# Kernel optimization log

Measured on AMD Instinct MI355X. Metric: run time of the kernel, lower is better.

## Reference

```python
import jax, jax.numpy as jnp
import numpy as np

B, L, C, H, K, P = 64, 2048, 128, 128, 64, 336
NUM_BLOCKS = 4
EPS = 1e-5


def _revin_norm(x):
    mean = jnp.mean(x, axis=1, keepdims=True)
    std = jnp.sqrt(jnp.var(x, axis=1, keepdims=True) + EPS)
    return (x - mean) / std, mean, std


def _bn(x, gamma, beta, ch_axis):
    # training-mode BatchNorm1d: stats over all axes except ch_axis
    axes = tuple(i for i in range(x.ndim) if i != ch_axis)
    mean = jnp.mean(x, axis=axes, keepdims=True)
    var = jnp.var(x, axis=axes, keepdims=True)
    shp = [1] * x.ndim
    shp[ch_axis] = -1
    return (x - mean) / jnp.sqrt(var + EPS) * gamma.reshape(shp) + beta.reshape(shp)


def _mixer_block(x, bn_t_g, bn_t_b, lin_t_w, lin_t_b, bn_f_g, bn_f_b,
                 lin_f1_w, lin_f1_b, lin_f2_w, lin_f2_b):
    # timestep mixer: BN treats seq dim as channels, Linear over seq dim
    y = _bn(x, bn_t_g, bn_t_b, 1)                       # [B,L,C]
    y = jnp.swapaxes(y, 1, 2)                           # [B,C,L]
    y = jax.nn.gelu(y @ lin_t_w + lin_t_b, approximate=False)
    y = jnp.swapaxes(y, 1, 2)
    x = x + y
    # feature mixer: BN over channel dim, 2-layer MLP over features
    y = jnp.swapaxes(x, 1, 2)                           # [B,C,L]
    y = _bn(y, bn_f_g, bn_f_b, 1)
    y = jnp.swapaxes(y, 1, 2)                           # [B,L,C]
    y = jax.nn.gelu(y @ lin_f1_w + lin_f1_b, approximate=False)
    y = y @ lin_f2_w + lin_f2_b
    return x + y


def _forward(x, bern_u, cluster_embeds, wq_w, wq_b, wk_w, wk_b, wv_w, wv_b,
             cm_w1, cm_b1, cm_w2, cm_b2, tm_w1, tm_b1, tm_w2, tm_b2,
             bn_t_g, bn_t_b, lin_t_w, lin_t_b, bn_f_g, bn_f_b,
             lin_f1_w, lin_f1_b, lin_f2_w, lin_f2_b, out_w, out_b):
    xn, _, _ = _revin_norm(x)                           # [B,L,C]
    # channel MLP -> token embeddings h_i
    h = jax.nn.relu(xn @ cm_w1 + cm_b1) @ cm_w2 + cm_b2  # [B,L,H]
    # cosine-similarity soft routing to codebook
    hn = h / (jnp.linalg.norm(h, axis=-1, keepdims=True) + 1e-8)
    cn = cluster_embeds / (jnp.linalg.norm(cluster_embeds, axis=-1, keepdims=True) + 1e-8)
    p = jax.nn.softmax(jnp.einsum('blh,kh->blk', hn, cn), axis=-1)   # [B,L,K]
    M = (bern_u < p).astype(x.dtype)                    # bernoulli sample via external uniforms
    # exp-attention between cluster queries and token keys, masked by M
    Q = cluster_embeds @ wq_w + wq_b                    # [K,H]
    Km = h @ wk_w + wk_b                                # [B,L,H]
    V = h @ wv_w + wv_b                                 # [B,L,H]
    scores = jnp.einsum('kh,blh->bkl', Q, Km) / jnp.sqrt(jnp.asarray(H, x.dtype))
    aw = jax.nn.softmax(jnp.exp(scores) * jnp.swapaxes(M, 1, 2), axis=-1)  # [B,K,L]
    ao = jnp.einsum('bkl,blh->bkh', aw, V)              # [B,K,H]
    upd = ao * jnp.mean(p, axis=1)[:, :, None]          # prob-weighted cluster update
    new_cluster_embeds = jnp.mean(upd, axis=0)          # [K,H] (EMA-style copy target)
    # temporal module on channel embeddings
    h2 = jax.nn.relu(h @ tm_w1 + tm_b1) @ tm_w2 + tm_b2  # [B,L,H], H==C
    z, mean2, std2 = _revin_norm(h2)                    # second 'norm' overwrites stats
    for _ in range(NUM_BLOCKS):
        z = _mixer_block(z, bn_t_g, bn_t_b, lin_t_w, lin_t_b,
                         bn_f_g, bn_f_b, lin_f1_w, lin_f1_b, lin_f2_w, lin_f2_b)
    y = jnp.swapaxes(jnp.swapaxes(z, 1, 2) @ out_w + out_b, 1, 2)    # [B,P,C]
    y = y * std2 + mean2                                # denorm with second-call stats
    return y, new_cluster_embeds


def setup_inputs() -> dict:
    key = jax.random.key(0)
    ks = iter(jax.random.split(key, 40))

    def lin_w(fan_in, shape):
        return jax.random.uniform(next(ks), shape, jnp.float32, -1.0, 1.0) / np.sqrt(fan_in).astype(np.float32)

    return {
        'x': jax.random.normal(next(ks), (B, L, C), jnp.float32),
        'bern_u': jax.random.uniform(next(ks), (B, L, K), jnp.float32),
        'cluster_embeds': jax.random.normal(next(ks), (K, H), jnp.float32),
        'wq_w': lin_w(H, (H, H)), 'wq_b': lin_w(H, (H,)),
        'wk_w': lin_w(H, (H, H)), 'wk_b': lin_w(H, (H,)),
        'wv_w': lin_w(H, (H, H)), 'wv_b': lin_w(H, (H,)),
        'cm_w1': lin_w(C, (C, H)), 'cm_b1': lin_w(C, (H,)),
        'cm_w2': lin_w(H, (H, H)), 'cm_b2': lin_w(H, (H,)),
        'tm_w1': lin_w(H, (H, H)), 'tm_b1': lin_w(H, (H,)),
        'tm_w2': lin_w(H, (H, H)), 'tm_b2': lin_w(H, (H,)),
        'bn_t_g': jnp.ones((L,), jnp.float32), 'bn_t_b': jnp.zeros((L,), jnp.float32),
        'lin_t_w': lin_w(L, (L, L)), 'lin_t_b': lin_w(L, (L,)),
        'bn_f_g': jnp.ones((C,), jnp.float32), 'bn_f_b': jnp.zeros((C,), jnp.float32),
        'lin_f1_w': lin_w(C, (C, H)), 'lin_f1_b': lin_w(C, (H,)),
        'lin_f2_w': lin_w(H, (H, C)), 'lin_f2_b': lin_w(H, (C,)),
        'out_w': lin_w(L, (L, P)), 'out_b': lin_w(L, (P,)),
    }


def reference(x, bern_u, cluster_embeds, wq_w, wq_b, wk_w, wk_b, wv_w, wv_b,
              cm_w1, cm_b1, cm_w2, cm_b2, tm_w1, tm_b1, tm_w2, tm_b2,
              bn_t_g, bn_t_b, lin_t_w, lin_t_b, bn_f_g, bn_f_b,
              lin_f1_w, lin_f1_b, lin_f2_w, lin_f2_b, out_w, out_b):
    return _forward(x, bern_u, cluster_embeds, wq_w, wq_b, wk_w, wk_b, wv_w, wv_b,
                    cm_w1, cm_b1, cm_w2, cm_b2, tm_w1, tm_b1, tm_w2, tm_b2,
                    bn_t_g, bn_t_b, lin_t_w, lin_t_b, bn_f_g, bn_f_b,
                    lin_f1_w, lin_f1_b, lin_f2_w, lin_f2_b, out_w, out_b)
```

## Files before the change

### kernel.cpp

```cpp
#include <hip/hip_runtime.h>
#include <math.h>

#define BB 64
#define LL 2048
#define CC 128
#define HH 128
#define KK 64
#define PP 336
#define EPSf 1e-5f

typedef __attribute__((ext_vector_type(8))) short short8v;
typedef __attribute__((ext_vector_type(4))) float float4v;

__device__ inline ushort f2bf(float f) {
    union { float f; unsigned u; } v; v.f = f;
    unsigned r = (v.u + 0x7FFFu + ((v.u >> 16) & 1u)) >> 16;
    return (ushort)r;
}
__device__ inline float bf2f(ushort h) {
    union { unsigned u; float f; } v; v.u = ((unsigned)h) << 16;
    return v.f;
}

__device__ inline float fast_gelu(float v) {
// ... 432 lines not shown
                    for (int nf = 0; nf < 4; ++nf)
                        acc2[mf][nf] = __builtin_amdgcn_mfma_f32_16x16x32_bf16(
                            ah[mf], bl[nf], acc2[mf][nf], 0, 0, 0);
                #pragma unroll
                for (int mf = 0; mf < 4; ++mf)
                    #pragma unroll
                    for (int nf = 0; nf < 4; ++nf)
                        acc2[mf][nf] = __builtin_amdgcn_mfma_f32_16x16x32_bf16(
                            al[mf], bh[nf], acc2[mf][nf], 0, 0, 0);
            }
        }
    }

    int rbase = kq * 4;
    float rs_[4][4];
    float rq_[4][4];
    float cs_[4], cq_[4];
    if (EP2 == 1 || EP2 == 3) {
        #pragma unroll
        for (int a = 0; a < 4; ++a)
            #pragma unroll
            for (int b = 0; b < 4; ++b) { rs_[a][b] = 0.f; rq_[a][b] = 0.f; }
    }
    if (EP2 == 2) {
        #pragma unroll
        for (int a = 0; a < 4; ++a) { cs_[a] = 0.f; cq_[a] = 0.f; }
    }
    #pragma unroll
    for (int nf = 0; nf < 4; ++nf) {
        int n = wn + nf * 16 + col;
        float bn = b2v[n];
        #pragma unroll
        for (int mf = 0; mf < 4; ++mf) {
            #pragma unroll
            for (int r = 0; r < 4; ++r) {
                int m = m0 + wm + mf * 16 + rbase + r;
                float v = acc2[mf][nf][r] + bn;
                if (ACT2 == 1) v = fmaxf(v, 0.f);
                if (ACT2 == 2) v = fast_gelu(v);
                if (EP2 == 1) {
                    float fin = Out[(size_t)m * 128 + n] + v;
                    Out[(size_t)m * 128 + n] = fin;
                    rs_[mf][r] += fin;
                    rq_[mf][r] += fin * fin;
                } else {
                    Out[(size_t)m * 128 + n] = v;
                    if (EP2 == 2) { cs_[nf] += v; cq_[nf] += v * v; }
                    if (EP2 == 3) rq_[mf][r] += v * v;
                }
            }
        }
    }
    if (EP2 == 1) {
        #pragma unroll
        for (int mf = 0; mf < 4; ++mf)
            #pragma unroll
            for (int r = 0; r < 4; ++r) {
                float s = rs_[mf][r], q = rq_[mf][r];
                #pragma unroll
                for (int o = 1; o <= 8; o <<= 1) {
                    s += __shfl_xor(s, o);
                    q += __shfl_xor(q, o);
                }
                rs_[mf][r] = s; rq_[mf][r] = q;
            }
        __syncthreads();
        float* sred = (float*)&Xhi[0][0];
        float* qred = sred + 256;
        if (col == 0) {
            #pragma unroll
            for (int mf = 0; mf < 4; ++mf)
                #pragma unroll
                for (int r = 0; r < 4; ++r) {
                    int row = wm + mf * 16 + kq * 4 + r;
                    sred[row * 2 + (wn >> 6)] = rs_[mf][r];
                    qred[row * 2 + (wn >> 6)] = rq_[mf][r];
                }
        }
        __syncthreads();
        if (tid < 128) {
            rsum[(size_t)m0 + tid] = sred[tid * 2] + sred[tid * 2 + 1];
            rsq[(size_t)m0 + tid]  = qred[tid * 2] + qred[tid * 2 + 1];
        }
    }
    if (EP2 == 3) {
        #pragma unroll
        for (int mf = 0; mf < 4; ++mf)
            #pragma unroll
            for (int r = 0; r < 4; ++r) {
                float q = rq_[mf][r];
                #pragma unroll
                for (int o = 1; o <= 8; o <<= 1) q += __shfl_xor(q, o);
                rq_[mf][r] = q;
            }
        __syncthreads();
        float* qred = (float*)&Xhi[0][0];
        if (col == 0) {
            #pragma unroll
            for (int mf = 0; mf < 4; ++mf)
                #pragma unroll
                for (int r = 0; r < 4; ++r) {
                    int row = wm + mf * 16 + kq * 4 + r;
                    qred[row * 2 + (wn >> 6)] = rq_[mf][r];
                }
        }
        __syncthreads();
        if (tid < 128)
            rsq[(size_t)m0 + tid] = qred[tid * 2] + qred[tid * 2 + 1];
    }
    if (EP2 == 2) {
        #pragma unroll
        for (int nf = 0; nf < 4; ++nf) {
            #pragma unroll
            for (int o = 16; o <= 32; o <<= 1) {
                cs_[nf] += __shfl_xor(cs_[nf], o);
                cq_[nf] += __shfl_xor(cq_[nf], o);
            }
        }
        __syncthreads();
        float* colS = (float*)&Xhi[0][0];
        float* colQ = colS + 256;
        if (kq == 0) {
            #pragma unroll
            for (int nf = 0; nf < 4; ++nf) {
                int n = wn + nf * 16 + col;
                colS[(wm >> 6) * 128 + n] = cs_[nf];
                colQ[(wm >> 6) * 128 + n] = cq_[nf];
            }
        }
        __syncthreads();
        if (tid < 128) {
            rsum[(size_t)blockIdx.x * 256 + tid] = colS[tid] + colS[128 + tid];
            rsum[(size_t)blockIdx.x * 256 + 128 + tid] = colQ[tid] + colQ[128 + tid];
        }
    }
}

__global__ void wsplit_kernel(const float* __restrict__ W, ushort* __restrict__ Whi,
                              ushort* __restrict__ Wlo) {
    __shared__ float t[32][33];
    int k0 = blockIdx.x * 32, n0 = blockIdx.y * 32;
    int tx = threadIdx.x, ty = threadIdx.y;
    for (int i = ty; i < 32; i += 8)
        t[i][tx] = W[(size_t)(k0 + i) * 128 + n0 + tx];
    __syncthreads();
    for (int i = ty; i < 32; i += 8) {
        float v = t[tx][i];
        ushort h = f2bf(v);
        Whi[(size_t)(n0 + i) * 128 + k0 + tx] = h;
        Wlo[(size_t)(n0 + i) * 128 + k0 + tx] = f2bf(v - bf2f(h));
    }
}

__global__ __launch_bounds__(512)
void mfma_ts_kernel(const ushort* __restrict__ A, const ushort* __restrict__ W,
                    const float* __restrict__ bias, float* Z,
                    int nx, int nwg, float* __restrict__ bnfP) {
    extern __shared__ __align__(16) ushort smem[];
    float (*Ol)[132] = (float(*)[132])smem;

    int bid = blockIdx.x;
    int cpx = nwg >> 3;
    int swz = (bid & 7) * cpx + (bid >> 3);
    int n0 = (swz % nx) * 128;
    int m0 = (swz / nx) * 128;

    int tid = threadIdx.x;
    int w = tid >> 6, lane = tid & 63;
    int wm = (w >> 1) * 32, wn = (w & 1) * 64;
    int col = lane & 15, kq = lane >> 4;
    int srow = lane >> 3;
    int scol = ((lane & 7) ^ srow) << 3;
    int xr = (col & 7) << 4;

    float4v acc[2][4];
    #pragma unroll
    for (int i = 0; i < 2; ++i)
        #pragma unroll
        for (int j = 0; j < 4; ++j) acc[i][j] = (float4v){0.f, 0.f, 0.f, 0.f};

    const int kTiles = LL >> 6;

    auto stage = [&](int kt2, int bsel) {
        ushort* Ab = smem + bsel * 16384;
        ushort* Bb = Ab + 8192;
        int kb = kt2 << 6;
        #pragma unroll
        for (int it = 0; it < 2; ++it) {
            int rb = w * 16 + it * 8;
            async16(A + (size_t)(m0 + rb + srow) * LL + kb + scol, Ab + (rb << 6));
            async16(W + (size_t)(n0 + rb + srow) * LL + kb + scol, Bb + (rb << 6));
        }
    };

    stage(0, 0);
    stage(1, 1);
    int cur = 0;
    for (int kt = 0; kt < kTiles; ++kt) {
        if (kt + 1 < kTiles)
            asm volatile("s_waitcnt vmcnt(4)" ::: "memory");
        else
            asm volatile("s_waitcnt vmcnt(0)" ::: "memory");
        __builtin_amdgcn_s_barrier();
        __builtin_amdgcn_sched_barrier(0);
        if (kt + 2 < kTiles) {
            int nb = cur + 2; if (nb >= 3) nb -= 3;
            stage(kt + 2, nb);
        }
        const ushort* Ac = smem + cur * 16384;
        const ushort* Bc = Ac + 8192;
        __builtin_amdgcn_s_setprio(1);
        #pragma unroll
        for (int ksub = 0; ksub < 2; ++ksub) {
            int cswz = (((ksub << 6) + (kq << 4)) ^ xr) >> 1;
            short8v af[2], bf[4];
            af[0] = *(const short8v*)(Ac + (wm + col) * 64 + cswz);
            af[1] = *(const short8v*)(Ac + (wm + 16 + col) * 64 + cswz);
            #pragma unroll
            for (int nf = 0; nf < 4; ++nf)
                bf[nf] = *(const short8v*)(Bc + (wn + nf * 16 + col) * 64 + cswz);
            #pragma unroll
            for (int mf = 0; mf < 2; ++mf)
                #pragma unroll
                for (int nf = 0; nf < 4; ++nf)
                    acc[mf][nf] = __builtin_amdgcn_mfma_f32_16x16x32_bf16(
                        af[mf], bf[nf], acc[mf][nf], 0, 0, 0);
        }
        __builtin_amdgcn_s_setprio(0);
        ++cur; if (cur == 3) cur = 0;
    }

    int b = m0 >> 7;
    float cs[8], cq[8];
    #pragma unroll
    for (int j = 0; j < 8; ++j) { cs[j] = 0.f; cq[j] = 0.f; }
    #pragma unroll
    for (int q = 0; q < 4; ++q) {
        __syncthreads();
        #pragma unroll
        for (int nf = 0; nf < 4; ++nf) {
            int gnl = wn + nf * 16;
            if ((gnl >> 5) != q) continue;
            int gn = n0 + gnl + col;
            float bn = bias[gn];
            int nl = gnl - q * 32 + col;
            #pragma unroll
            for (int mf = 0; mf < 2; ++mf)
                #pragma unroll
                for (int r = 0; r < 4; ++r) {
                    float v = acc[mf][nf][r] + bn;
                    v = fast_gelu(v);
                    Ol[nl][wm + mf * 16 + kq * 4 + r] = v;
                }
        }
        __syncthreads();
        int nloc = tid >> 4, c0 = (tid & 15) * 8;
        int gn = n0 + q * 32 + nloc;
        float* zr = Z + ((size_t)b * LL + gn) * CC + c0;
        #pragma unroll
        for (int i = 0; i < 2; ++i) {
            float4 v = *(float4*)&Ol[nloc][c0 + i * 4];
            float4 o = *(float4*)(zr + i * 4);
            v.x += o.x; v.y += o.y; v.z += o.z; v.w += o.w;
            *(float4*)(zr + i * 4) = v;
            cs[i * 4 + 0] += v.x; cs[i * 4 + 1] += v.y;
            cs[i * 4 + 2] += v.z; cs[i * 4 + 3] += v.w;
            cq[i * 4 + 0] += v.x * v.x; cq[i * 4 + 1] += v.y * v.y;
            cq[i * 4 + 2] += v.z * v.z; cq[i * 4 + 3] += v.w * v.w;
        }
    }
    __syncthreads();
    float* sred = (float*)smem;
    float* qred = sred + 4096;
    int rrow = tid >> 4, cb = (tid & 15) * 8;
    #pragma unroll
    for (int j = 0; j < 8; ++j) {
        sred[rrow * 128 + cb + j] = cs[j];
        qred[rrow * 128 + cb + j] = cq[j];
    }
    __syncthreads();
    if (tid < 128) {
        float a = 0.f;
        for (int r = 0; r < 32; ++r) a += sred[r * 128 + tid];
        bnfP[(size_t)bid * 256 + tid] = a;
    } else if (tid < 256) {
        int c = tid - 128;
        float a = 0.f;
        for (int r = 0; r < 32; ++r) a += qred[r * 128 + c];
        bnfP[(size_t)bid * 256 + 128 + c] = a;
    }
}

template <int EPM>
__global__ __launch_bounds__(256)
void mfma_gemm_kernel(const ushort* __restrict__ A, const ushort* __restrict__ W,
                      const float* __restrict__ bias, float* Z,
                      int N, int Kd, int LDO, int nx, int nwg,
                      const float* __restrict__ epS, const float* __restrict__ epM,
                      float* __restrict__ bnfP) {
    __shared__ __align__(16) ushort smem[32768];
    float (*Ol)[132] = (float(*)[132])smem;

    int bid = blockIdx.x;
    int cpx = nwg >> 3;
    int swz = (bid & 7) * cpx + (bid >> 3);
    int n0 = (swz % nx) * 128;
    int m0 = (swz / nx) * 128;

    int tid = threadIdx.x;
    int w = tid >> 6, lane = tid & 63;
    int wm = (w >> 1) * 64, wn = (w & 1) * 64;
    int col = lane & 15, kq = lane >> 4;

    int srow = lane >> 3;
    int scol = ((lane & 7) ^ srow) << 3;
    int xr = (col & 7) << 4;

    float4v acc[4][4];
    #pragma unroll
    for (int i = 0; i < 4; ++i)
        #pragma unroll
        for (int j = 0; j < 4; ++j) acc[i][j] = (float4v){0.f, 0.f, 0.f, 0.f};

    int kTiles = Kd >> 6;

    #pragma unroll
    for (int it = 0; it < 4; ++it) {
        int rb = (w << 5) + (it << 3);
        async16(A + (size_t)(m0 + rb + srow) * Kd + scol, smem + (rb << 6));
    }
    #pragma unroll
    for (int it = 0; it < 4; ++it) {
        int rb = (w << 5) + (it << 3);
        async16(W + (size_t)(n0 + rb + srow) * Kd + scol, smem + 8192 + (rb << 6));
    }
    __syncthreads();

    for (int kt = 0; kt < kTiles; ++kt) {
        int cur = kt & 1;
        ushort* Ac = smem + (cur << 14);
        ushort* Bc = Ac + 8192;
        if (kt + 1 < kTiles) {
            ushort* An = smem + ((cur ^ 1) << 14);
            ushort* Bn = An + 8192;
            int kb = (kt + 1) << 6;
            #pragma unroll
            for (int it = 0; it < 4; ++it) {
                int rb = (w << 5) + (it << 3);
                async16(A + (size_t)(m0 + rb + srow) * Kd + kb + scol, An + (rb << 6));
            }
            #pragma unroll
            for (int it = 0; it < 4; ++it) {
                int rb = (w << 5) + (it << 3);
                async16(W + (size_t)(n0 + rb + srow) * Kd + kb + scol, Bn + (rb << 6));
            }
        }
        __builtin_amdgcn_s_setprio(1);
        #pragma unroll
        for (int ksub = 0; ksub < 2; ++ksub) {
            int cswz = (((ksub << 6) + (kq << 4)) ^ xr) >> 1;
            short8v af[4], bf[4];
            #pragma unroll
            for (int mf = 0; mf < 4; ++mf)
                af[mf] = *(const short8v*)(Ac + (wm + mf * 16 + col) * 64 + cswz);
            #pragma unroll
            for (int nf = 0; nf < 4; ++nf)
                bf[nf] = *(const short8v*)(Bc + (wn + nf * 16 + col) * 64 + cswz);
            #pragma unroll
            for (int mf = 0; mf < 4; ++mf)
                #pragma unroll
                for (int nf = 0; nf < 4; ++nf)
                    acc[mf][nf] = __builtin_amdgcn_mfma_f32_16x16x32_bf16(
                        af[mf], bf[nf], acc[mf][nf], 0, 0, 0);
        }
        __builtin_amdgcn_s_setprio(0);
        __syncthreads();
    }

    int b = m0 >> 7;
    float cs[16], cq[16];
    if (EPM == 1) {
        #pragma unroll
        for (int k2 = 0; k2 < 16; ++k2) { cs[k2] = 0.f; cq[k2] = 0.f; }
    }
    #pragma unroll
    for (int q = 0; q < 4; ++q) {
        __syncthreads();
        #pragma unroll
        for (int nf = 0; nf < 4; ++nf) {
            int gnl = wn + nf * 16;
            if ((gnl >> 5) != q) continue;
            int gn = n0 + gnl + col;
            float bn = (EPM == 2 && gn >= N) ? 0.f : bias[gn];
            int nl = gnl - q * 32 + col;
            #pragma unroll
            for (int mf = 0; mf < 4; ++mf) {
                #pragma unroll
                for (int r = 0; r < 4; ++r) {
                    float v = acc[mf][nf][r] + bn;
                    if (EPM == 1) v = fast_gelu(v);
                    Ol[nl][wm + mf * 16 + kq * 4 + r] = v;
                }
            }
        }
        __syncthreads();
        int nloc = tid >> 3, c0 = (tid & 7) * 16;
        int gn = n0 + q * 32 + nloc;
        if ((EPM == 2 || EPM == 3) && gn >= N) continue;
        float* zr;
        if (EPM == 3)
            zr = Z + (((size_t)(m0 >> 11) * 64 + gn) * 2048) + (m0 & 2047) + c0;
        else
            zr = Z + ((size_t)b * LDO + gn) * CC + c0;
        #pragma unroll
        for (int i = 0; i < 4; ++i) {
            float4 v = *(float4*)&Ol[nloc][c0 + i * 4];
            if (EPM == 1) {
                float4 o = *(float4*)(zr + i * 4);
                v.x += o.x; v.y += o.y; v.z += o.z; v.w += o.w;
                *(float4*)(zr + i * 4) = v;
                cs[i * 4 + 0] += v.x; cs[i * 4 + 1] += v.y;
                cs[i * 4 + 2] += v.z; cs[i * 4 + 3] += v.w;
                cq[i * 4 + 0] += v.x * v.x; cq[i * 4 + 1] += v.y * v.y;
                cq[i * 4 + 2] += v.z * v.z; cq[i * 4 + 3] += v.w * v.w;
            } else if (EPM == 2) {
                int mb = m0 + c0 + i * 4;
                float4 s4 = *(const float4*)(epS + mb);
                float4 m4 = *(const float4*)(epM + mb);
                v.x = v.x * s4.x + m4.x; v.y = v.y * s4.y + m4.y;
                v.z = v.z * s4.z + m4.z; v.w = v.w * s4.w + m4.w;
                *(float4*)(zr + i * 4) = v;
            } else {
                *(float4*)(zr + i * 4) = v;
            }
        }
    }
    if (EPM == 1) {
        __syncthreads();
        float* sred = (float*)smem;
        float* qred = sred + 4096;
        int rrow = tid >> 3, cb = (tid & 7) * 16;
// ... 161 lines not shown
void awh_part_kernel(const float* __restrict__ AWs, const float* __restrict__ hmat,
                     float* __restrict__ part) {
    __shared__ float AT[32][64];
    __shared__ float VT[32][128];
    int b = blockIdx.y, sp = blockIdx.x;
    int tid = threadIdx.x;
    int tx = tid & 15, ty = tid >> 4;
    float acc[4][8] = {};
    const float* Ab = AWs + (size_t)b * KK * LL + sp * 512;
    const float* Vb = hmat + ((size_t)b * LL + sp * 512) * HH;
    for (int lt = 0; lt < 512; lt += 32) {
        __syncthreads();
        #pragma unroll
        for (int it = 0; it < 2; ++it) {
            int q = tid + it * 256;
            int row = q >> 3;
            int lq = (q & 7) << 2;
            float4 v = *(const float4*)(Ab + (size_t)row * LL + lt + lq);
            AT[lq][row] = v.x; AT[lq + 1][row] = v.y;
            AT[lq + 2][row] = v.z; AT[lq + 3][row] = v.w;
        }
        #pragma unroll
        for (int it = 0; it < 4; ++it) {
            int q = tid + it * 256;
            int lr = q >> 5;
            int hc = (q & 31) << 2;
            *(float4*)&VT[lr][hc] = *(const float4*)(Vb + (size_t)(lt + lr) * HH + hc);
        }
        __syncthreads();
        #pragma unroll
        for (int l = 0; l < 32; ++l) {
            float av[4], vv[8];
            *(float4*)&av[0] = *(const float4*)&AT[l][ty * 4];
            *(float4*)&vv[0] = *(const float4*)&VT[l][tx * 4];
            *(float4*)&vv[4] = *(const float4*)&VT[l][64 + tx * 4];
            #pragma unroll
            for (int i = 0; i < 4; ++i)
                #pragma unroll
                for (int j = 0; j < 8; ++j)
                    acc[i][j] = fmaf(av[i], vv[j], acc[i][j]);
        }
    }
    #pragma unroll
    for (int i = 0; i < 4; ++i) {
        int k = ty * 4 + i;
        #pragma unroll
        for (int jj = 0; jj < 8; jj += 4) {
            int h = (jj ? 64 + tx * 4 : tx * 4);
            float o[4];
            #pragma unroll
            for (int j = 0; j < 4; ++j) o[j] = acc[i][jj + j];
            *(float4*)(part + (((size_t)b * 4 + sp) * KK + k) * HH + h) = *(float4*)o;
        }
    }
}

__global__ void awh_reduce_kernel(const float* __restrict__ part, float* __restrict__ awh) {
    int bk = blockIdx.x, h = threadIdx.x;
    int b = bk >> 6, k = bk & 63;
    float s = 0.f;
    #pragma unroll
    for (int sp = 0; sp < 4; ++sp)
        s += part[(((size_t)b * 4 + sp) * KK + k) * HH + h];
    awh[(size_t)bk * HH + h] = s;
}

__global__ void newce_kernel(const float* __restrict__ ao, const float* __restrict__ pm,
                             float* __restrict__ outTail) {
    int k = blockIdx.x, h = threadIdx.x;
    float s = 0.f;
    for (int b = 0; b < BB; ++b)
        s += ao[((size_t)b * KK + k) * HH + h] * pm[b * KK + k];
    outTail[(size_t)k * HH + h] = s * (1.f / BB);
}

__global__ void revin_apply_kernel(const float* __restrict__ in, float* __restrict__ out,
                                   const float* __restrict__ mu, const float* __restrict__ rs,
                                   float* __restrict__ rsum, float* __restrict__ rsq) {
    int b = blockIdx.y;
    size_t base = (size_t)b * LL * CC + (size_t)blockIdx.x * 8192;
    int c0 = (threadIdx.x * 4) & 127;
    int lane = threadIdx.x & 63;
    float4 m4 = *(const float4*)(mu + b * CC + c0);
    float4 r4 = *(const float4*)(rs + b * CC + c0);
    #pragma unroll
    for (int j = 0; j < 8; ++j) {
        float4 v = *(const float4*)(in + base + threadIdx.x * 4 + j * 1024);
        v.x = (v.x - m4.x) * r4.x; v.y = (v.y - m4.y) * r4.y;
        v.z = (v.z - m4.z) * r4.z; v.w = (v.w - m4.w) * r4.w;
        *(float4*)(out + base + threadIdx.x * 4 + j * 1024) = v;
        float s = v.x + v.y + v.z + v.w;
        float q = v.x * v.x + v.y * v.y + v.z * v.z + v.w * v.w;
        #pragma unroll
        for (int o = 1; o <= 16; o <<= 1) {
            s += __shfl_xor(s, o);
            q += __shfl_xor(q, o);
        }
        if ((lane & 31) == 0) {
            size_t row = (base + (size_t)threadIdx.x * 4 + (size_t)j * 1024) >> 7;
            rsum[row] = s;
            rsq[row] = q;
        }
    }
}

__global__ void bnt_final_kernel(const float* __restrict__ rsum, const float* __restrict__ rsq,
                                 float* __restrict__ mu, float* __restrict__ rv) {
    int l = blockIdx.x * 256 + threadIdx.x;
    float s = 0.f, q = 0.f;
    for (int b = 0; b < BB; ++b) {
        s += rsum[(size_t)b * LL + l];
        q += rsq[(size_t)b * LL + l];
    }
    float m = s * (1.f / (BB * CC));
    float var = q * (1.f / (BB * CC)) - m * m;
    var = fmaxf(var, 0.f);
    mu[l] = m;
    rv[l] = 1.f / sqrtf(var + EPSf);
}

template <bool DO_BN>
__global__ __launch_bounds__(256)
void transpose_bn_kernel(const float* __restrict__ in, ushort* __restrict__ out,
                         const float* __restrict__ mu, const float* __restrict__ rv,
                         const float* __restrict__ g, const float* __restrict__ be) {
    __shared__ ushort tile[32][72];
    int l0 = blockIdx.x * 64, c0 = blockIdx.y * 32, b = blockIdx.z;
    int t = threadIdx.x;
    const float* ib = in + ((size_t)b * LL + l0) * CC + c0;
    #pragma unroll
    for (int it = 0; it < 2; ++it) {
        int idx = t + it * 256;
        int row = idx >> 3;
        int c = (idx & 7) * 4;
        float4 v = *(const float4*)(ib + (size_t)row * CC + c);
        if (DO_BN) {
            int l = l0 + row;
            float sc = rv[l] * g[l];
            float m = mu[l], bb = be[l];
            v.x = (v.x - m) * sc + bb; v.y = (v.y - m) * sc + bb;
            v.z = (v.z - m) * sc + bb; v.w = (v.w - m) * sc + bb;
        }
        tile[c    ][row] = f2bf(v.x);
        tile[c + 1][row] = f2bf(v.y);
        tile[c + 2][row] = f2bf(v.z);
        tile[c + 3][row] = f2bf(v.w);
    }
    __syncthreads();
    int cc = t >> 3, l8 = (t & 7) * 8;
    ushort* ob = out + (size_t)b * CC * LL + (size_t)(c0 + cc) * LL + l0 + l8;
    *(uint4*)ob = *(const uint4*)&tile[cc][l8];
}

__global__ void bnf_mid_kernel(const float* __restrict__ part, float* __restrict__ mid) {
    int gblk = blockIdx.x, t = threadIdx.x;
    float s = 0.f;
    #pragma unroll
    for (int i = 0; i < 16; ++i)
        s += part[(size_t)(gblk * 16 + i) * 256 + t];
    mid[(size_t)gblk * 256 + t] = s;
}

__global__ void bnf_final_kernel(const float* __restrict__ mid, const float* __restrict__ g,
                                 const float* __restrict__ be, float* __restrict__ mu,
                                 float* __restrict__ sA, float* __restrict__ tA) {
    int c = threadIdx.x;
    float s = 0.f, s2 = 0.f;
    #pragma unroll
    for (int i = 0; i < 64; ++i) {
        s += mid[(size_t)i * 256 + c];
        s2 += mid[(size_t)i * 256 + 128 + c];
    }
    float m = s / (float)(BB * LL);
    float var = s2 / (float)(BB * LL) - m * m;
    var = fmaxf(var, 0.f);
    float rvv = 1.f / sqrtf(var + EPSf);
    mu[c] = m;
    sA[c] = rvv * g[c];
    tA[c] = be[c];
}

extern "C" void kernel_launch(void* const* d_in, const int* in_sizes, int n_in,
                              void* d_out, int out_size, void* d_ws, size_t ws_size,
                              hipStream_t stream) {
    const float* x     = (const float*)d_in[0];
    const float* bern  = (const float*)d_in[1];
    const float* ce    = (const float*)d_in[2];
    const float* wq_w  = (const float*)d_in[3];
    const float* wq_b  = (const float*)d_in[4];
    const float* wk_w  = (const float*)d_in[5];
    const float* wk_b  = (const float*)d_in[6];
    const float* wv_w  = (const float*)d_in[7];
    const float* wv_b  = (const float*)d_in[8];
    const float* cm_w1 = (const float*)d_in[9];
    const float* cm_b1 = (const float*)d_in[10];
    const float* cm_w2 = (const float*)d_in[11];
    const float* cm_b2 = (const float*)d_in[12];
    const float* tm_w1 = (const float*)d_in[13];
    const float* tm_b1 = (const float*)d_in[14];
    const float* tm_w2 = (const float*)d_in[15];
    const float* tm_b2 = (const float*)d_in[16];
    const float* bn_t_g = (const float*)d_in[17];
    const float* bn_t_b = (const float*)d_in[18];
    const float* lin_t_w = (const float*)d_in[19];
    const float* lin_t_b = (const float*)d_in[20];
    const float* bn_f_g = (const float*)d_in[21];
    const float* bn_f_b = (const float*)d_in[22];
    const float* f1_w  = (const float*)d_in[23];
    const float* f1_b  = (const float*)d_in[24];
    const float* f2_w  = (const float*)d_in[25];
    const float* f2_b  = (const float*)d_in[26];
    const float* out_w = (const float*)d_in[27];
    const float* out_b = (const float*)d_in[28];
    (void)in_sizes; (void)n_in; (void)out_size;

    float* y = (float*)d_out;
    float* ceOut = y + (size_t)BB * PP * CC;

    float* ws = (float*)d_ws;
    size_t off = 0;
    auto alloc = [&](size_t n) { float* p = ws + off; off += n; return p; };
    float* mean1  = alloc(BB * CC);
    float* rstd1  = alloc(BB * CC);
    float* std1   = alloc(BB * CC);
    float* mean2  = alloc(BB * CC);
    float* rstd2  = alloc(BB * CC);
    float* std2   = alloc(BB * CC);
    float* bnmu   = alloc(LL);
    float* bnrv   = alloc(LL);
    float* bfpart = alloc(1024 * 256);
    float* bfmid  = alloc(64 * 256);
    float* bfmu   = alloc(CC);
    float* bfs    = alloc(CC);
    float* bft    = alloc(CC);
    float* cxpart = alloc(BB * 8 * 256);
    float* cpart2 = alloc(1024 * 256);
    float* qbuf   = alloc(KK * HH);
    ushort* qpb   = (ushort*)alloc(128 * 128 / 2);
    float* qbp    = alloc(128);
    ushort* cnbh  = (ushort*)alloc(8192);
    ushort* cnbl  = (ushort*)alloc(8192);
    float* rn     = alloc((size_t)BB * LL);
    float* rsum   = alloc((size_t)BB * LL);
    float* rsq    = alloc((size_t)BB * LL);
    float* ppart  = alloc((size_t)BB * (LL / 32) * KK);
    float* pmean  = alloc(BB * KK);
    float* awhprt = alloc((size_t)BB * 4 * KK * HH);
    float* awh    = alloc((size_t)BB * KK * HH);
    float* aobuf  = alloc((size_t)BB * KK * HH);
    ushort* wsp   = (ushort*)alloc(7 * 2 * 16384 / 2);
    ushort* wtT   = (ushort*)alloc((size_t)LL * LL / 2);
    ushort* owT   = (ushort*)alloc((size_t)384 * LL / 2);
    float* S      = alloc((size_t)BB * KK * LL);
    float* buf0   = alloc((size_t)BB * LL * CC);
    float* buf2   = alloc((size_t)BB * LL * CC);
    unsigned char* Mt = (unsigned char*)(ws + off);
    ushort* abf = (ushort*)S;
    ushort* hb  = (ushort*)buf0;
    (void)ws_size;

    auto whi = [&](int i) { return wsp + (size_t)i * 2 * 16384; };
    auto wlo = [&](int i) { return wsp + (size_t)i * 2 * 16384 + 16384; };

    const int ML = BB * LL;
    dim3 tb(32, 8);
    dim3 tgrid(LL / 64, CC / 32, BB);
    dim3 wsg(4, 4);

    bool useTs =
        (hipFuncSetAttribute((const void*)mfma_ts_kernel,
                             hipFuncAttributeMaxDynamicSharedMemorySize,
                             98304) == hipSuccess);

    wtrans_kernel<<<dim3(LL / 32, LL / 32), tb, 0, stream>>>(lin_t_w, wtT, LL, LL);
    wtrans_kernel<<<dim3(LL / 32, 12), tb, 0, stream>>>(out_w, owT, LL, PP);
    wsplit_kernel<<<wsg, tb, 0, stream>>>(cm_w1, whi(0), wlo(0));
    wsplit_kernel<<<wsg, tb, 0, stream>>>(cm_w2, whi(1), wlo(1));
    wsplit_kernel<<<wsg, tb, 0, stream>>>(tm_w1, whi(2), wlo(2));
    wsplit_kernel<<<wsg, tb, 0, stream>>>(tm_w2, whi(3), wlo(3));
    wsplit_kernel<<<wsg, tb, 0, stream>>>(f1_w, whi(4), wlo(4));
    wsplit_kernel<<<wsg, tb, 0, stream>>>(f2_w, whi(5), wlo(5));
    wsplit_kernel<<<wsg, tb, 0, stream>>>(wv_w, whi(6), wlo(6));

    colstats_part_kernel<<<dim3(8, BB), 256, 0, stream>>>(x, cxpart);
    colstats_final_kernel<<<dim3(BB), dim3(128), 0, stream>>>(cxpart, mean1, rstd1, std1);
    mfma_sq2_kernel<1, 1, 0, 3, 1><<<dim3(ML / 128), 256, 0, stream>>>(
        x, whi(0), wlo(0), cm_b1, whi(1), wlo(1), cm_b2, buf2, mean1, rstd1, nullptr, CC,
        nullptr, rsq);
    rn_final_kernel<<<dim3(ML / 256), 256, 0, stream>>>(rsq, rn);
    gemm_kernel<<<dim3(1, 1), 256, 0, stream>>>(ce, wq_w, wq_b, qbuf,
        KK, HH, HH, HH, HH, HH);
    qprime_kernel<<<dim3(128), dim3(128), 0, stream>>>(qbuf, wk_w, wk_b, qpb, qbp);
    cn_split_kernel<<<dim3(128), dim3(128), 0, stream>>>(ce, cnbh, cnbl);
    mfma_sq_kernel<0, 0, 2><<<dim3(ML / 128), 256, 0, stream>>>(
        buf2, cnbh, cnbl, nullptr, S, nullptr, nullptr, nullptr, 0, hb);
    pmask_kernel<<<dim3(LL / 32, BB), 256, 0, stream>>>(S, rn, bern, Mt, ppart);
    pmean_final_kernel<<<dim3(BB), dim3(64), 0, stream>>>(ppart, pmean);
    mfma_gemm_kernel<3><<<dim3(1024), 256, 0, stream>>>(
        hb, qpb, qbp, S, KK, 128, 0, 1, 1024, nullptr, nullptr, nullptr);
    aw_kernel<<<dim3(BB * KK), 256, 0, stream>>>(S, Mt);
    awh_part_kernel<<<dim3(4, BB), 256, 0, stream>>>(S, buf2, awhprt);
    awh_reduce_kernel<<<dim3(BB * KK), dim3(128), 0, stream>>>(awhprt, awh);
    mfma_sq_kernel<0, 0, 0><<<dim3((BB * KK) / 128), 256, 0, stream>>>(
        awh, whi(6), wlo(6), wv_b, aobuf, nullptr, nullptr, nullptr, 0, nullptr);
    newce_kernel<<<dim3(KK), dim3(128), 0, stream>>>(aobuf, pmean, ceOut);
    mfma_sq2_kernel<0, 1, 0, 2, 1><<<dim3(ML / 128), 256, 0, stream>>>(
        buf2, whi(2), wlo(2), tm_b1, whi(3), wlo(3), tm_b2, buf0,
        nullptr, nullptr, nullptr, 0, cpart2, nullptr);
    colstats2_final_kernel<<<dim3(BB), dim3(128), 0, stream>>>(cpart2, mean2, rstd2, std2);
    revin_apply_kernel<<<dim3(32, BB), 256, 0, stream>>>(buf0, buf2, mean2, rstd2, rsum, rsq);
    for (int blkI = 0; blkI < 4; ++blkI) {
        bnt_final_kernel<<<dim3(8), 256, 0, stream>>>(rsum, rsq, bnmu, bnrv);
        transpose_bn_kernel<true><<<tgrid, 256, 0, stream>>>(buf2, abf, bnmu, bnrv, bn_t_g, bn_t_b);
        if (useTs)
            mfma_ts_kernel<<<dim3(1024), 512, 98304, stream>>>(
                abf, wtT, lin_t_b, buf2, 16, 1024, bfpart);
        else
            mfma_gemm_kernel<1><<<dim3(1024), 256, 0, stream>>>(
                abf, wtT, lin_t_b, buf2, LL, LL, LL, 16, 1024, nullptr, nullptr, bfpart);
        bnf_mid_kernel<<<dim3(64), 256, 0, stream>>>(bfpart, bfmid);
        bnf_final_kernel<<<dim3(1), dim3(128), 0, stream>>>(bfmid, bn_f_g, bn_f_b, bfmu, bfs, bft);
        mfma_sq2_kernel<2, 2, 0, 1, 0><<<dim3(ML / 128), 256, 0, stream>>>(
            buf2, whi(4), wlo(4), f1_b, whi(5), wlo(5), f2_b, buf2, bfmu, bfs, bft, 0,
            rsum, rsq);
    }
    transpose_bn_kernel<false><<<tgrid, 256, 0, stream>>>(buf2, abf,
        nullptr, nullptr, nullptr, nullptr);
    mfma_gemm_kernel<2><<<dim3(192), 256, 0, stream>>>(
        abf, owT, out_b, y, PP, LL, PP, 3, 192, std2, mean2, nullptr);
}
```

Before: 1.338 ms.

## Enlarge timestep-mixer GEMM tile to 256x256 with double buffering

Replaces the 128x128 tile timestep-mixer MFMA kernel (1024 workgroups, triple-buffered async loads with vmcnt waits) with a 256x256 tile kernel (256 workgroups, 8 waves, 128x64 per wave) that uses simple double buffering and a full barrier each k-step. Larger tiles raise arithmetic intensity and cut global/LDS traffic per FLOP. The epilogue now spans two batches per tile and the BN-feature partial reduction count changes. The cost is 128 accumulator floats per lane (register pressure, one block per CU), only 256 workgroups for 256 CUs, and a less overlapped pipeline.

```diff
diff --git a/kernel.cpp b/kernel.cpp
--- a/kernel.cpp
+++ b/kernel.cpp
@@ -608,90 +608,83 @@
     }
 }
 
-__global__ __launch_bounds__(512)
-void mfma_ts_kernel(const ushort* __restrict__ A, const ushort* __restrict__ W,
-                    const float* __restrict__ bias, float* Z,
-                    int nx, int nwg, float* __restrict__ bnfP) {
-    extern __shared__ __align__(16) ushort smem[];
-    float (*Ol)[132] = (float(*)[132])smem;
+__global__ __launch_bounds__(512, 1)
+void mfma_ts2_kernel(const ushort* __restrict__ A, const ushort* __restrict__ W,
+                     const float* __restrict__ bias, float* Z,
+                     float* __restrict__ bnfP) {
+    extern __shared__ __align__(16) ushort smem2[];
+    float (*Ol)[260] = (float(*)[260])smem2;
 
     int bid = blockIdx.x;
-    int cpx = nwg >> 3;
-    int swz = (bid & 7) * cpx + (bid >> 3);
-    int n0 = (swz % nx) * 128;
-    int m0 = (swz / nx) * 128;
+    int swz = (bid & 7) * 32 + (bid >> 3);
+    int n0 = (swz & 7) * 256;
+    int m0 = (swz >> 3) * 256;
 
     int tid = threadIdx.x;
     int w = tid >> 6, lane = tid & 63;
-    int wm = (w >> 1) * 32, wn = (w & 1) * 64;
+    int wm = (w >> 2) * 128, wn = (w & 3) * 64;
     int col = lane & 15, kq = lane >> 4;
     int srow = lane >> 3;
     int scol = ((lane & 7) ^ srow) << 3;
     int xr = (col & 7) << 4;
 
-    float4v acc[2][4];
-    #pragma unroll
-    for (int i = 0; i < 2; ++i)
+    float4v acc[8][4];
+    #pragma unroll
+    for (int i = 0; i < 8; ++i)
         #pragma unroll
         for (int j = 0; j < 4; ++j) acc[i][j] = (float4v){0.f, 0.f, 0.f, 0.f};
 
-    const int kTiles = LL >> 6;
-
+    const int kTiles = 32;
     auto stage = [&](int kt2, int bsel) {
-        ushort* Ab = smem + bsel * 16384;
-        ushort* Bb = Ab + 8192;
+        ushort* Ab = smem2 + bsel * 32768;
+        ushort* Bb = Ab + 16384;
         int kb = kt2 << 6;
         #pragma unroll
-        for (int it = 0; it < 2; ++it) {
-            int rb = w * 16 + it * 8;
+        for (int it = 0; it < 4; ++it) {
+            int rb = w * 32 + it * 8;
             async16(A + (size_t)(m0 + rb + srow) * LL + kb + scol, Ab + (rb << 6));
             async16(W + (size_t)(n0 + rb + srow) * LL + kb + scol, Bb + (rb << 6));
         }
     };
 
     stage(0, 0);
-    stage(1, 1);
-    int cur = 0;
+    __syncthreads();
     for (int kt = 0; kt < kTiles; ++kt) {
-        if (kt + 1 < kTiles)
-            asm volatile("s_waitcnt vmcnt(4)" ::: "memory");
-        else
-            asm volatile("s_waitcnt vmcnt(0)" ::: "memory");
-        __builtin_amdgcn_s_barrier();
-        __builtin_amdgcn_sched_barrier(0);
-        if (kt + 2 < kTiles) {
-            int nb = cur + 2; if (nb >= 3) nb -= 3;
-            stage(kt + 2, nb);
-        }
-        const ushort* Ac = smem + cur * 16384;
-        const ushort* Bc = Ac + 8192;
+        int cur = kt & 1;
+        const ushort* Ac = smem2 + cur * 32768;
+        const ushort* Bc = Ac + 16384;
+        if (kt + 1 < kTiles) stage(kt + 1, cur ^ 1);
         __builtin_amdgcn_s_setprio(1);
         #pragma unroll
         for (int ksub = 0; ksub < 2; ++ksub) {
             int cswz = (((ksub << 6) + (kq << 4)) ^ xr) >> 1;
-            short8v af[2], bf[4];
-            af[0] = *(const short8v*)(Ac + (wm + col) * 64 + cswz);
-            af[1] = *(const short8v*)(Ac + (wm + 16 + col) * 64 + cswz);
+            short8v af[8], bf[4];
+            #pragma unroll
+            for (int mf = 0; mf < 8; ++mf)
+                af[mf] = *(const short8v*)(Ac + (wm + mf * 16 + col) * 64 + cswz);
             #pragma unroll
             for (int nf = 0; nf < 4; ++nf)
                 bf[nf] = *(const short8v*)(Bc + (wn + nf * 16 + col) * 64 + cswz);
             #pragma unroll
-            for (int mf = 0; mf < 2; ++mf)
+            for (int mf = 0; mf < 8; ++mf)
                 #pragma unroll
                 for (int nf = 0; nf < 4; ++nf)
                     acc[mf][nf] = __builtin_amdgcn_mfma_f32_16x16x32_bf16(
                         af[mf], bf[nf], acc[mf][nf], 0, 0, 0);
         }
         __builtin_amdgcn_s_setprio(0);
-        ++cur; if (cur == 3) cur = 0;
-    }
-
-    int b = m0 >> 7;
-    float cs[8], cq[8];
-    #pragma unroll
-    for (int j = 0; j < 8; ++j) { cs[j] = 0.f; cq[j] = 0.f; }
-    #pragma unroll
-    for (int q = 0; q < 4; ++q) {
+        __syncthreads();
+    }
+
+    int b0 = m0 >> 7;
+    float cs[16], cq[16];
+    #pragma unroll
+    for (int j = 0; j < 16; ++j) { cs[j] = 0.f; cq[j] = 0.f; }
+    int nloc = tid >> 4, c0 = (tid & 15) * 16;
+    int bb = b0 + (c0 >> 7);
+    int ccc = c0 & 127;
+    #pragma unroll
+    for (int q = 0; q < 8; ++q) {
         __syncthreads();
         #pragma unroll
         for (int nf = 0; nf < 4; ++nf) {
@@ -701,7 +694,7 @@
             float bn = bias[gn];
             int nl = gnl - q * 32 + col;
             #pragma unroll
-            for (int mf = 0; mf < 2; ++mf)
+            for (int mf = 0; mf < 8; ++mf)
                 #pragma unroll
                 for (int r = 0; r < 4; ++r) {
                     float v = acc[mf][nf][r] + bn;
@@ -710,11 +703,10 @@
                 }
         }
         __syncthreads();
-        int nloc = tid >> 4, c0 = (tid & 15) * 8;
         int gn = n0 + q * 32 + nloc;
-        float* zr = Z + ((size_t)b * LL + gn) * CC + c0;
-        #pragma unroll
-        for (int i = 0; i < 2; ++i) {
+        float* zr = Z + ((size_t)bb * LL + gn) * CC + ccc;
+        #pragma unroll
+        for (int i = 0; i < 4; ++i) {
             float4 v = *(float4*)&Ol[nloc][c0 + i * 4];
             float4 o = *(float4*)(zr + i * 4);
             v.x += o.x; v.y += o.y; v.z += o.z; v.w += o.w;
@@ -726,23 +718,24 @@
         }
     }
     __syncthreads();
-    float* sred = (float*)smem;
-    float* qred = sred + 4096;
-    int rrow = tid >> 4, cb = (tid & 15) * 8;
-    #pragma unroll
-    for (int j = 0; j < 8; ++j) {
-        sred[rrow * 128 + cb + j] = cs[j];
-        qred[rrow * 128 + cb + j] = cq[j];
+    float* sred = (float*)smem2;
+    float* qred = sred + 8192;
+    #pragma unroll
+    for (int j = 0; j < 16; ++j) {
+        sred[nloc * 256 + c0 + j] = cs[j];
+        qred[nloc * 256 + c0 + j] = cq[j];
     }
     __syncthreads();
     if (tid < 128) {
         float a = 0.f;
-        for (int r = 0; r < 32; ++r) a += sred[r * 128 + tid];
+        for (int r = 0; r < 32; ++r)
+            a += sred[r * 256 + tid] + sred[r * 256 + 128 + tid];
         bnfP[(size_t)bid * 256 + tid] = a;
     } else if (tid < 256) {
         int c = tid - 128;
         float a = 0.f;
-        for (int r = 0; r < 32; ++r) a += qred[r * 128 + c];
+        for (int r = 0; r < 32; ++r)
+            a += qred[r * 256 + c] + qred[r * 256 + 128 + c];
         bnfP[(size_t)bid * 256 + 128 + c] = a;
     }
 }
@@ -1210,12 +1203,12 @@
     *(uint4*)ob = *(const uint4*)&tile[cc][l8];
 }
 
-__global__ void bnf_mid_kernel(const float* __restrict__ part, float* __restrict__ mid) {
+__global__ void bnf_mid_kernel(const float* __restrict__ part, float* __restrict__ mid,
+                               int cnt) {
     int gblk = blockIdx.x, t = threadIdx.x;
     float s = 0.f;
-    #pragma unroll
-    for (int i = 0; i < 16; ++i)
-        s += part[(size_t)(gblk * 16 + i) * 256 + t];
+    for (int i = 0; i < cnt; ++i)
+        s += part[(size_t)(gblk * cnt + i) * 256 + t];
     mid[(size_t)gblk * 256 + t] = s;
 }
 
@@ -1325,10 +1318,10 @@
     dim3 tgrid(LL / 64, CC / 32, BB);
     dim3 wsg(4, 4);
 
-    bool useTs =
-        (hipFuncSetAttribute((const void*)mfma_ts_kernel,
+    bool useTs2 =
+        (hipFuncSetAttribute((const void*)mfma_ts2_kernel,
                              hipFuncAttributeMaxDynamicSharedMemorySize,
-                             98304) == hipSuccess);
+                             131072) == hipSuccess);
 
     wtrans_kernel<<<dim3(LL / 32, LL / 32), tb, 0, stream>>>(lin_t_w, wtT, LL, LL);
     wtrans_kernel<<<dim3(LL / 32, 12), tb, 0, stream>>>(out_w, owT, LL, PP);
@@ -1370,13 +1363,15 @@
     for (int blkI = 0; blkI < 4; ++blkI) {
         bnt_final_kernel<<<dim3(8), 256, 0, stream>>>(rsum, rsq, bnmu, bnrv);
         transpose_bn_kernel<true><<<tgrid, 256, 0, stream>>>(buf2, abf, bnmu, bnrv, bn_t_g, bn_t_b);
-        if (useTs)
-            mfma_ts_kernel<<<dim3(1024), 512, 98304, stream>>>(
-                abf, wtT, lin_t_b, buf2, 16, 1024, bfpart);
-        else
+        if (useTs2) {
+            mfma_ts2_kernel<<<dim3(256), 512, 131072, stream>>>(
+                abf, wtT, lin_t_b, buf2, bfpart);
+            bnf_mid_kernel<<<dim3(64), 256, 0, stream>>>(bfpart, bfmid, 4);
+        } else {
             mfma_gemm_kernel<1><<<dim3(1024), 256, 0, stream>>>(
                 abf, wtT, lin_t_b, buf2, LL, LL, LL, 16, 1024, nullptr, nullptr, bfpart);
-        bnf_mid_kernel<<<dim3(64), 256, 0, stream>>>(bfpart, bfmid);
+            bnf_mid_kernel<<<dim3(64), 256, 0, stream>>>(bfpart, bfmid, 16);
+        }
         bnf_final_kernel<<<dim3(1), dim3(128), 0, stream>>>(bfmid, bn_f_g, bn_f_b, bfmu, bfs, bft);
         mfma_sq2_kernel<2, 2, 0, 1, 0><<<dim3(ML / 128), 256, 0, stream>>>(
             buf2, whi(4), wlo(4), f1_b, whi(5), wlo(5), f2_b, buf2, bfmu, bfs, bft, 0,
```

New measurement: 1.357 ms. Within noise of the previous version (+1.5%).

## Replace 8-wave triple-buffered timestep GEMM with 4-wave double-buffered 64x64-per-wave kernel

Applied to the files above, without the earlier changes.

The timestep-mixer GEMM kernel moves from 512 threads with 96KB of dynamic LDS, triple buffering and 64-wide K tiles to 256 threads with 32KB of static LDS, double buffering and 32-wide K tiles. Each wave now computes a 64x64 output tile with a 4x4 MFMA fragment grid instead of 32x64, which raises register reuse of the A/B fragments. The smaller LDS footprint should allow more workgroups per CU. In exchange, pipeline depth drops to one tile ahead, each K step is half as deep with a full barrier per iteration, accumulator register pressure rises, and the LDS swizzle changes. The epilogue mapping and stats reduction are adjusted for the 256-thread layout.

```diff
diff --git a/kernel.cpp b/kernel.cpp
--- a/kernel.cpp
+++ b/kernel.cpp
@@ -608,11 +608,11 @@
     }
 }
 
-__global__ __launch_bounds__(512)
-void mfma_ts_kernel(const ushort* __restrict__ A, const ushort* __restrict__ W,
-                    const float* __restrict__ bias, float* Z,
-                    int nx, int nwg, float* __restrict__ bnfP) {
-    extern __shared__ __align__(16) ushort smem[];
+__global__ __launch_bounds__(256)
+void mfma_ts4_kernel(const ushort* __restrict__ A, const ushort* __restrict__ W,
+                     const float* __restrict__ bias, float* Z,
+                     int nx, int nwg, float* __restrict__ bnfP) {
+    __shared__ __align__(16) ushort smem[16384];
     float (*Ol)[132] = (float(*)[132])smem;
 
     int bid = blockIdx.x;
@@ -623,73 +623,68 @@
 
     int tid = threadIdx.x;
     int w = tid >> 6, lane = tid & 63;
-    int wm = (w >> 1) * 32, wn = (w & 1) * 64;
+    int wm = (w >> 1) * 64, wn = (w & 1) * 64;
     int col = lane & 15, kq = lane >> 4;
-    int srow = lane >> 3;
-    int scol = ((lane & 7) ^ srow) << 3;
-    int xr = (col & 7) << 4;
-
-    float4v acc[2][4];
-    #pragma unroll
-    for (int i = 0; i < 2; ++i)
+
+    int srow = lane >> 2;
+    int sj = lane & 3;
+    int su = (sj ^ ((srow >> 1) & 3)) * 8;
+    int uo = (kq ^ ((col >> 1) & 3)) * 8;
+
+    float4v acc[4][4];
+    #pragma unroll
+    for (int i = 0; i < 4; ++i)
         #pragma unroll
         for (int j = 0; j < 4; ++j) acc[i][j] = (float4v){0.f, 0.f, 0.f, 0.f};
 
-    const int kTiles = LL >> 6;
-
-    auto stage = [&](int kt2, int bsel) {
-        ushort* Ab = smem + bsel * 16384;
-        ushort* Bb = Ab + 8192;
-        int kb = kt2 << 6;
-        #pragma unroll
-        for (int it = 0; it < 2; ++it) {
-            int rb = w * 16 + it * 8;
-            async16(A + (size_t)(m0 + rb + srow) * LL + kb + scol, Ab + (rb << 6));
-            async16(W + (size_t)(n0 + rb + srow) * LL + kb + scol, Bb + (rb << 6));
-        }
-    };
-
-    stage(0, 0);
-    stage(1, 1);
-    int cur = 0;
+    const int Kd = LL;
+    const int kTiles = 64;
+
+    #pragma unroll
+    for (int it = 0; it < 2; ++it) {
+        int R = w * 32 + it * 16;
+        async16(A + (size_t)(m0 + R + srow) * Kd + su, smem + R * 32);
+        async16(W + (size_t)(n0 + R + srow) * Kd + su, smem + 4096 + R * 32);
+    }
+    __syncthreads();
+
     for (int kt = 0; kt < kTiles; ++kt) {
-        if (kt + 1 < kTiles)
-            asm volatile("s_waitcnt vmcnt(4)" ::: "memory");
-        else
-            asm volatile("s_waitcnt vmcnt(0)" ::: "memory");
-        __builtin_amdgcn_s_barrier();
-        __builtin_amdgcn_sched_barrier(0);
-        if (kt + 2 < kTiles) {
-            int nb = cur + 2; if (nb >= 3) nb -= 3;
-            stage(kt + 2, nb);
-        }
-        const ushort* Ac = smem + cur * 16384;
-        const ushort* Bc = Ac + 8192;
+        int cur = kt & 1;
+        const ushort* Ac = smem + (cur << 13);
+        const ushort* Bc = Ac + 4096;
+        if (kt + 1 < kTiles) {
+            ushort* An = smem + ((cur ^ 1) << 13);
+            ushort* Bn = An + 4096;
+            int kb = (kt + 1) << 5;
+            #pragma unroll
+            for (int it = 0; it < 2; ++it) {
+                int R = w * 32 + it * 16;
+                async16(A + (size_t)(m0 + R + srow) * Kd + kb + su, An + R * 32);
+                async16(W + (size_t)(n0 + R + srow) * Kd + kb + su, Bn + R * 32);
+            }
+        }
         __builtin_amdgcn_s_setprio(1);
-        #pragma unroll
-        for (int ksub = 0; ksub < 2; ++ksub) {
-            int cswz = (((ksub << 6) + (kq << 4)) ^ xr) >> 1;
-            short8v af[2], bf[4];
-            af[0] = *(const short8v*)(Ac + (wm + col) * 64 + cswz);
-            af[1] = *(const short8v*)(Ac + (wm + 16 + col) * 64 + cswz);
+        short8v af[4], bf[4];
+        #pragma unroll
+        for (int mf = 0; mf < 4; ++mf)
+            af[mf] = *(const short8v*)(Ac + (wm + mf * 16 + col) * 32 + uo);
+        #pragma unroll
+        for (int nf = 0; nf < 4; ++nf)
+            bf[nf] = *(const short8v*)(Bc + (wn + nf * 16 + col) * 32 + uo);
+        #pragma unroll
+        for (int mf = 0; mf < 4; ++mf)
             #pragma unroll
             for (int nf = 0; nf < 4; ++nf)
-                bf[nf] = *(const short8v*)(Bc + (wn + nf * 16 + col) * 64 + cswz);
-            #pragma unroll
-            for (int mf = 0; mf < 2; ++mf)
-                #pragma unroll
-                for (int nf = 0; nf < 4; ++nf)
-                    acc[mf][nf] = __builtin_amdgcn_mfma_f32_16x16x32_bf16(
-                        af[mf], bf[nf], acc[mf][nf], 0, 0, 0);
-        }
+                acc[mf][nf] = __builtin_amdgcn_mfma_f32_16x16x32_bf16(
+                    af[mf], bf[nf], acc[mf][nf], 0, 0, 0);
         __builtin_amdgcn_s_setprio(0);
-        ++cur; if (cur == 3) cur = 0;
+        __syncthreads();
     }
 
     int b = m0 >> 7;
-    float cs[8], cq[8];
-    #pragma unroll
-    for (int j = 0; j < 8; ++j) { cs[j] = 0.f; cq[j] = 0.f; }
+    float cs[16], cq[16];
+    #pragma unroll
+    for (int k2 = 0; k2 < 16; ++k2) { cs[k2] = 0.f; cq[k2] = 0.f; }
     #pragma unroll
     for (int q = 0; q < 4; ++q) {
         __syncthreads();
@@ -701,20 +696,21 @@
             float bn = bias[gn];
             int nl = gnl - q * 32 + col;
             #pragma unroll
-            for (int mf = 0; mf < 2; ++mf)
+            for (int mf = 0; mf < 4; ++mf) {
                 #pragma unroll
                 for (int r = 0; r < 4; ++r) {
                     float v = acc[mf][nf][r] + bn;
                     v = fast_gelu(v);
                     Ol[nl][wm + mf * 16 + kq * 4 + r] = v;
                 }
-        }
-        __syncthreads();
-        int nloc = tid >> 4, c0 = (tid & 15) * 8;
+            }
+        }
+        __syncthreads();
+        int nloc = tid >> 3, c0 = (tid & 7) * 16;
         int gn = n0 + q * 32 + nloc;
         float* zr = Z + ((size_t)b * LL + gn) * CC + c0;
         #pragma unroll
-        for (int i = 0; i < 2; ++i) {
+        for (int i = 0; i < 4; ++i) {
             float4 v = *(float4*)&Ol[nloc][c0 + i * 4];
             float4 o = *(float4*)(zr + i * 4);
             v.x += o.x; v.y += o.y; v.z += o.z; v.w += o.w;
@@ -728,18 +724,18 @@
     __syncthreads();
     float* sred = (float*)smem;
     float* qred = sred + 4096;
-    int rrow = tid >> 4, cb = (tid & 15) * 8;
-    #pragma unroll
-    for (int j = 0; j < 8; ++j) {
-        sred[rrow * 128 + cb + j] = cs[j];
-        qred[rrow * 128 + cb + j] = cq[j];
+    int rrow = tid >> 3, cb = (tid & 7) * 16;
+    #pragma unroll
+    for (int k2 = 0; k2 < 16; ++k2) {
+        sred[rrow * 128 + cb + k2] = cs[k2];
+        qred[rrow * 128 + cb + k2] = cq[k2];
     }
     __syncthreads();
     if (tid < 128) {
         float a = 0.f;
         for (int r = 0; r < 32; ++r) a += sred[r * 128 + tid];
         bnfP[(size_t)bid * 256 + tid] = a;
-    } else if (tid < 256) {
+    } else {
         int c = tid - 128;
         float a = 0.f;
         for (int r = 0; r < 32; ++r) a += qred[r * 128 + c];
@@ -1325,11 +1321,6 @@
     dim3 tgrid(LL / 64, CC / 32, BB);
     dim3 wsg(4, 4);
 
-    bool useTs =
-        (hipFuncSetAttribute((const void*)mfma_ts_kernel,
-                             hipFuncAttributeMaxDynamicSharedMemorySize,
-                             98304) == hipSuccess);
-
     wtrans_kernel<<<dim3(LL / 32, LL / 32), tb, 0, stream>>>(lin_t_w, wtT, LL, LL);
     wtrans_kernel<<<dim3(LL / 32, 12), tb, 0, stream>>>(out_w, owT, LL, PP);
     wsplit_kernel<<<wsg, tb, 0, stream>>>(cm_w1, whi(0), wlo(0));
@@ -1370,12 +1361,8 @@
     for (int blkI = 0; blkI < 4; ++blkI) {
         bnt_final_kernel<<<dim3(8), 256, 0, stream>>>(rsum, rsq, bnmu, bnrv);
         transpose_bn_kernel<true><<<tgrid, 256, 0, stream>>>(buf2, abf, bnmu, bnrv, bn_t_g, bn_t_b);
-        if (useTs)
-            mfma_ts_kernel<<<dim3(1024), 512, 98304, stream>>>(
-                abf, wtT, lin_t_b, buf2, 16, 1024, bfpart);
-        else
-            mfma_gemm_kernel<1><<<dim3(1024), 256, 0, stream>>>(
-                abf, wtT, lin_t_b, buf2, LL, LL, LL, 16, 1024, nullptr, nullptr, bfpart);
+        mfma_ts4_kernel<<<dim3(1024), 256, 0, stream>>>(
+            abf, wtT, lin_t_b, buf2, 16, 1024, bfpart);
         bnf_mid_kernel<<<dim3(64), 256, 0, stream>>>(bfpart, bfmid);
         bnf_final_kernel<<<dim3(1), dim3(128), 0, stream>>>(bfmid, bn_f_g, bn_f_b, bfmu, bfs, bft);
         mfma_sq2_kernel<2, 2, 0, 1, 0><<<dim3(ML / 128), 256, 0, stream>>>(
```

Result: faster. 1.279 ms (-4.4%).
